# Optimization experiments

Hardware: AMD Instinct MI355X
Metric: run time of the kernel (lower is better)

## Reference

```python
import math
import jax, jax.numpy as jnp
import numpy as np

NUM_HEADS = 32
HEAD_DIM = 128
POOL = 16
MAX_REL = 8192
RMS_EPS = 1e-6


def _central_mask_features(distances, feature_size, seq_length):
    # center_widths = arange(F) + geomspace(1, seq_length-F+1, F, endpoint=False)
    log_end = math.log(float(seq_length - feature_size + 1))
    log_step = log_end / feature_size
    exponents = jnp.arange(feature_size, dtype=jnp.float32) * log_step
    center_widths = jnp.arange(feature_size, dtype=jnp.float32) + jnp.exp(exponents)
    return (center_widths > distances[..., None]).astype(jnp.float32)


def _shift(x, query_length, key_length):
    # x: [..., n_rows, n_diags] with n_diags = 2*n_rows
    batch_shape = x.shape[:-2]
    n_rows, n_diags = x.shape[-2], x.shape[-1]
    x = x.reshape(*batch_shape, n_diags, n_rows)
    x = x[..., 1:, :]
    x = x.reshape(*batch_shape, n_rows, n_diags - 1)
    return x[..., :key_length]


def setup_inputs() -> dict:
    key = jax.random.key(0)
    ks = jax.random.split(key, 12)
    B, S, D = 1, 8192, 1536
    HD = NUM_HEADS * HEAD_DIM  # 4096
    s = 0.02
    return {
        "x": jax.random.normal(ks[0], (B, S, D), jnp.float32),
        "w_rms": jnp.ones((D,), jnp.float32),
        "W_q": jax.random.normal(ks[1], (D, HD), jnp.float32) * s,
        "W_k": jax.random.normal(ks[2], (D, HD), jnp.float32) * s,
        "W_pos": jax.random.normal(ks[3], (2 * NUM_HEADS, HD), jnp.float32) * s,
        "b_pos": jnp.zeros((HD,), jnp.float32),
        "q_r_bias": jax.random.normal(ks[4], (1, 1, NUM_HEADS, HEAD_DIM), jnp.float32) * s,
        "k_r_bias": jax.random.normal(ks[5], (1, 1, NUM_HEADS, HEAD_DIM), jnp.float32) * s,
        "W_yq": jax.random.normal(ks[6], (D, HEAD_DIM), jnp.float32) * s,
        "W_yk": jax.random.normal(ks[7], (D, HEAD_DIM), jnp.float32) * s,
        "W_pair": jax.random.normal(ks[8], (NUM_HEADS, HEAD_DIM), jnp.float32) * s,
        "b_pair": jnp.zeros((HEAD_DIM,), jnp.float32),
    }


def reference(x, w_rms, W_q, W_k, W_pos, b_pos, q_r_bias, k_r_bias, W_yq, W_yk, W_pair, b_pair):
    B, S, D = x.shape
    Sp = S // POOL
    # mean-pool along sequence (kernel=stride=16)
    x_pooled = x.reshape(B, Sp, POOL, D).mean(axis=2)
    # RMSNorm
    x_norm = x_pooled * jax.lax.rsqrt(jnp.mean(x_pooled * x_pooled, axis=-1, keepdims=True) + RMS_EPS) * w_rms

    q = (x_norm @ W_q).reshape(B, Sp, NUM_HEADS, HEAD_DIM)
    k = (x_norm @ W_k).reshape(B, Sp, NUM_HEADS, HEAD_DIM)

    # relative-position features
    range_vec = jnp.arange(-Sp, Sp, dtype=jnp.float32)
    pos_feat = _central_mask_features(jnp.abs(range_vec), NUM_HEADS, MAX_REL // POOL)  # [2Sp, H]
    sign = jnp.sign(range_vec)[:, None]
    pos_feat = jnp.concatenate([pos_feat, sign * pos_feat], axis=-1)  # [2Sp, 2H]
    pos_enc = (pos_feat @ W_pos + b_pos).reshape(2 * Sp, NUM_HEADS, HEAD_DIM)

    term_q = jnp.einsum('bqhc,phc->bhqp', q + q_r_bias, pos_enc)
    term_k = jnp.einsum('bkhc,phc->bhkp', k + k_r_bias, pos_enc)
    rel_q_a = _shift(term_q, Sp, Sp)  # [B,H,Q,K]
    rel_k_a = _shift(term_k, Sp, Sp)
    rel_q_a = jnp.transpose(rel_q_a, (0, 2, 3, 1))  # [B,Q,K,H]
    rel_k_a = jnp.transpose(rel_k_a, (0, 3, 2, 1))  # [B,P,K,H]

    a = jnp.einsum('bqhc,bkhc->bqkh', q, k)
    a = a + 0.5 * (rel_q_a + rel_k_a)

    x_gelu = jax.nn.gelu(x_norm, approximate=False)
    y_q = x_gelu @ W_yq  # [B,Sp,HEAD_DIM]
    y_k = x_gelu @ W_yk

    pair_act = a @ W_pair + b_pair + y_q[:, :, None, :] + y_k[:, None, :, :]
    return pair_act
```

## Files before the change

kernel.cpp:

```cpp
#include <hip/hip_runtime.h>
#include <hip/hip_bf16.h>
#include <math.h>
#include <stdint.h>

#define NHEADS 32
#define HDIM 128
#define POOLW 16
#define DMODEL 1536
#define SPOOL 512
#define HDTOT 4096
#define PEROWS 1024
#define NPAIR (SPOOL * SPOOL)
#define TCOLS 80

typedef __hip_bfloat16 bf16;
typedef short short8 __attribute__((ext_vector_type(8)));
typedef float f32x4 __attribute__((ext_vector_type(4)));

__device__ __forceinline__ float b2f(const bf16 v) { return __bfloat162float(v); }
__device__ __forceinline__ bf16 f2b(float v) { return __float2bfloat16(v); }
__device__ __forceinline__ short f2bs(float v) {
  bf16 b = __float2bfloat16(v);
  return *reinterpret_cast<short*>(&b);
}

__device__ __forceinline__ void gload_lds16(const void* g, void* l) {
  const __attribute__((address_space(1))) uint32_t* gp =
      (const __attribute__((address_space(1))) uint32_t*)(uintptr_t)g;
  __attribute__((address_space(3))) uint32_t* lp =
      (__attribute__((address_space(3))) uint32_t*)(uintptr_t)l;
  __builtin_amdgcn_global_load_lds(gp, lp, 16, 0, 0);
}

__global__ __launch_bounds__(256) void pool_rms_gelu_bf(
    const float* __restrict__ x, const float* __restrict__ w_rms,
    bf16* __restrict__ xn, bf16* __restrict__ xg) {
  int sp = blockIdx.x;
  int tid = threadIdx.x;
  __shared__ float buf[DMODEL];
  __shared__ float red[256];
  const float* xrow = x + (size_t)sp * POOLW * DMODEL;
  float ss = 0.f;
  for (int d = tid; d < DMODEL; d += 256) {
    float s = 0.f;
#pragma unroll
    for (int p = 0; p < POOLW; ++p) s += xrow[p * DMODEL + d];
    s *= (1.0f / POOLW);
    buf[d] = s;
    ss += s * s;
  }
  red[tid] = ss;
  __syncthreads();
  for (int off = 128; off > 0; off >>= 1) {
    if (tid < off) red[tid] += red[tid + off];
    __syncthreads();
  }
  float rms = rsqrtf(red[0] / DMODEL + 1e-6f);
  for (int d = tid; d < DMODEL; d += 256) {
    float v = buf[d] * rms * w_rms[d];
    xn[(size_t)sp * DMODEL + d] = f2b(v);
    xg[(size_t)sp * DMODEL + d] = f2b(0.5f * v * (1.0f + erff(v * 0.70710678118654752f)));
  }
}

__global__ __launch_bounds__(256) void suffix_kernel(
    const float* __restrict__ W_pos, float* __restrict__ SW0, float* __restrict__ SW1) {
  int j = blockIdx.x * 256 + threadIdx.x;
  float s0 = 0.f, s1 = 0.f;
  SW0[32 * HDTOT + j] = 0.f;
  SW1[32 * HDTOT + j] = 0.f;
  for (int f = 31; f >= 0; --f) {
    s0 += W_pos[f * HDTOT + j];
    s1 += W_pos[(NHEADS + f) * HDTOT + j];
    SW0[f * HDTOT + j] = s0;
    SW1[f * HDTOT + j] = s1;
  }
}

__global__ __launch_bounds__(256) void prep_kernel(
    const float* __restrict__ SW0, const float* __restrict__ SW1,
    const float* __restrict__ b_pos, const float* __restrict__ qrb,
    const float* __restrict__ krb, bf16* __restrict__ SWb,
    float* __restrict__ RB, short* __restrict__ fm_tab) {
  int b = blockIdx.x, t = threadIdx.x;
  if (b < 32) {
    int h = b;
    bf16* dst = SWb + (size_t)h * 128 * 128;
    for (int rr = 0; rr < 128; rr += 2) {
      int g = rr + (t >> 7);
      int c = t & 127;
      float v;
      if (g < 33) v = SW0[(size_t)g * HDTOT + h * 128 + c];
      else if (g < 66) v = SW1[(size_t)(g - 33) * HDTOT + h * 128 + c];
      else if (g == 66) v = b_pos[h * 128 + c];
      else v = 0.f;
      dst[(size_t)g * 128 + c] = f2b(v);
    }
  } else if (b < 96) {
    int idx = b - 32;
    int s = idx >> 5, h = idx & 31;
    const float* rb = (s ? krb : qrb) + h * 128;
    if (t < 128) {
      int g = t;
      float acc = 0.f;
      if (g < 33) { for (int c = 0; c < 128; ++c) acc += rb[c] * SW0[(size_t)g * HDTOT + h * 128 + c]; }
      else if (g < 66) { for (int c = 0; c < 128; ++c) acc += rb[c] * SW1[(size_t)(g - 33) * HDTOT + h * 128 + c]; }
      else if (g == 66) { for (int c = 0; c < 128; ++c) acc += rb[c] * b_pos[h * 128 + c]; }
      RB[(size_t)idx * 128 + g] = acc;
    }
  } else {
    for (int p = t; p < 1024; p += 256) {
      float dist = fabsf((float)(p - 512));
      double ls = log(481.0) / 32.0;
      int fmv = 0;
      for (int f = 0; f < 32; ++f) {
        float cw = (float)f + expf((float)f * (float)ls);
        if (cw <= dist) fmv = f + 1;
      }
      fm_tab[p] = (short)fmv;
    }
  }
}

__global__ __launch_bounds__(256) void transpose_cast(
    const float* __restrict__ in, bf16* __restrict__ out, int R, int C) {
  __shared__ float tile[32][33];
  int c0 = blockIdx.x * 32, r0 = blockIdx.y * 32;
  int tx = threadIdx.x & 31, ty = threadIdx.x >> 5;
  for (int i = ty; i < 32; i += 8) tile[i][tx] = in[(size_t)(r0 + i) * C + c0 + tx];
  __syncthreads();
  for (int i = ty; i < 32; i += 8) out[(size_t)(c0 + i) * R + r0 + tx] = f2b(tile[tx][i]);
}

__global__ __launch_bounds__(256) void gemm_mfma(
    const bf16* __restrict__ A, int lda, long long batchA,
    const bf16* __restrict__ BT, int ldb, long long batchB,
    void* __restrict__ C, int ldc, long long batchC,
    const float* __restrict__ extra, int mode, int M, int N, int K) {
  __shared__ short Asub[128][32];
  __shared__ short Bsub[64][32];
  const int t = threadIdx.x;
  const int lane = t & 63;
  const int w = t >> 6;
  const int m0 = blockIdx.y * 128, n0 = blockIdx.x * 64;
  const int wm = (w >> 1) * 64, wn = (w & 1) * 32;
  const bf16* Ag = A + (size_t)blockIdx.z * batchA;
  const bf16* Bg = BT + (size_t)blockIdx.z * batchB;

  const int ar0 = t >> 2;
  const int as0 = t & 3;
  const int ao0 = as0 ^ (ar0 & 3);
  char* AsubB = (char*)&Asub[0][0];
  char* BsubB = (char*)&Bsub[0][0];
  char* ldsA0 = AsubB + w * 1024;
  char* ldsA1 = AsubB + 4096 + w * 1024;
  char* ldsB0 = BsubB + w * 1024;

  const int quad = lane >> 4, mr = lane & 15;
  f32x4 acc[4][2];
#pragma unroll
  for (int mi = 0; mi < 4; ++mi)
#pragma unroll
    for (int ni = 0; ni < 2; ++ni) acc[mi][ni] = (f32x4){0.f, 0.f, 0.f, 0.f};

  for (int k0 = 0; k0 < K; k0 += 32) {
    gload_lds16(Ag + (size_t)(m0 + ar0) * lda + k0 + ao0 * 8, ldsA0);
    gload_lds16(Ag + (size_t)(m0 + 64 + ar0) * lda + k0 + ao0 * 8, ldsA1);
    gload_lds16(Bg + (size_t)(n0 + ar0) * ldb + k0 + ao0 * 8, ldsB0);
    __syncthreads();
    short8 af[4];
#pragma unroll
    for (int mi = 0; mi < 4; ++mi) {
      int r = wm + mi * 16 + mr;
      af[mi] = *(const short8*)&Asub[r][(quad ^ (r & 3)) * 8];
    }
    short8 bfr[2];
#pragma unroll
    for (int ni = 0; ni < 2; ++ni) {
      int r = wn + ni * 16 + mr;
      bfr[ni] = *(const short8*)&Bsub[r][(quad ^ (r & 3)) * 8];
    }
#pragma unroll
    for (int mi = 0; mi < 4; ++mi)
#pragma unroll
      for (int ni = 0; ni < 2; ++ni)
        acc[mi][ni] = __builtin_amdgcn_mfma_f32_16x16x32_bf16(af[mi], bfr[ni], acc[mi][ni], 0, 0, 0);
    __syncthreads();
  }

  size_t cbase = (size_t)blockIdx.z * batchC;
#pragma unroll
  for (int mi = 0; mi < 4; ++mi) {
#pragma unroll
    for (int ni = 0; ni < 2; ++ni) {
#pragma unroll
      for (int r = 0; r < 4; ++r) {
        int gm = m0 + wm + mi * 16 + quad * 4 + r;
        int gn = n0 + wn + ni * 16 + mr;
        float v = acc[mi][ni][r];
        if (mode == 0) {
          ((float*)C)[cbase + (size_t)gm * ldc + gn] = v;
        } else if (mode == 1) {
          ((bf16*)C)[cbase + (size_t)gm * ldc + gn] = f2b(v);
        } else {
          if (gn < TCOLS) {
            ((float*)C)[cbase + (size_t)gm * ldc + gn] =
                v + extra[blockIdx.z * 128 + gn];
          }
        }
      }
    }
  }
}

#define MEGA_LDS 145536
__global__ __launch_bounds__(512) void mega_kernel(
    const bf16* __restrict__ QKp, const float* __restrict__ Tg,
    const short* __restrict__ fm_tab, const bf16* __restrict__ WpT,
    const float* __restrict__ b_pair, const float* __restrict__ yqk,
    float* __restrict__ out) {
  extern __shared__ char sm[];
  short* Qs = (short*)(sm);
  short* Ks = (short*)(sm + 8192);
  float* Ssc = (float*)(sm + 57344);
  short* fmL = (short*)(sm + 61568);
  short* Pl = (short*)(sm + 63616);

  const int t = threadIdx.x;
  const int lane = t & 63, w = t >> 6;
  const int quad = lane >> 4, mr = lane & 15;
  const int q0 = (blockIdx.x >> 4) * 32;
  const int k0 = (blockIdx.x & 15) * 32;

  const int c_ks = t >> 7;
  const int c_cc = t & 127;
  const int c_r = c_cc >> 2;
  const int c_pc = c_cc & 3;
  const int qk_col = c_ks * 32 + ((c_pc ^ (c_r & 3)) * 8);
  const int t_r0 = t / 20, t_p0 = t - t_r0 * 20;
  const int c2 = 512 + t;
  const int t_r1 = c2 / 20, t_p1 = c2 - t_r1 * 20;

#define STAGE_QK(h)                                                                   \
  {                                                                                   \
    gload_lds16(QKp + (size_t)(q0 + c_r) * 8192 + (h)*128 + qk_col, (char*)Qs + t * 16); \
    gload_lds16(QKp + (size_t)(k0 + c_r) * 8192 + 4096 + (h)*128 + qk_col,            \
                (char*)Ks + t * 16);                                                  \
  }
#define STAGE_T(h)                                                                    \
  {                                                                                   \
    char* dq = sm + 16384 + ((h)&1) * 10240;                                          \
    char* dk = sm + 36864 + ((h)&1) * 10240;                                          \
    const float* sq_ = Tg + (size_t)(h)*512 * TCOLS;                                  \
    const float* sk_ = Tg + (size_t)(32 + (h)) * 512 * TCOLS;                         \
    gload_lds16(sq_ + (size_t)(q0 + t_r0) * TCOLS + t_p0 * 4, dq + t * 16);           \
    gload_lds16(sk_ + (size_t)(k0 + t_r0) * TCOLS + t_p0 * 4, dk + t * 16);           \
    if (t < 128) {                                                                    \
      gload_lds16(sq_ + (size_t)(q0 + t_r1) * TCOLS + t_p1 * 4, dq + c2 * 16);        \
      gload_lds16(sk_ + (size_t)(k0 + t_r1) * TCOLS + t_p1 * 4, dk + c2 * 16);        \
    }                                                                                 \
  }

  if (t < 128) gload_lds16(fm_tab + t * 8, (char*)fmL + t * 16);
  STAGE_QK(0);
  STAGE_T(0);
  __syncthreads();

  for (int h = 0; h < 32; ++h) {
    if (w < 4) {
      const int smi = w >> 1, sni = w & 1;
      const int ra = smi * 16 + mr, rb = sni * 16 + mr;
      f32x4 accS = (f32x4){0.f, 0.f, 0.f, 0.f};
#pragma unroll
      for (int ks = 0; ks < 4; ++ks) {
        short8 af = *(const short8*)&Qs[ks * 1024 + ra * 32 + ((quad ^ (ra & 3)) * 8)];
        short8 bfv = *(const short8*)&Ks[ks * 1024 + rb * 32 + ((quad ^ (rb & 3)) * 8)];
        accS = __builtin_amdgcn_mfma_f32_16x16x32_bf16(af, bfv, accS, 0, 0, 0);
      }
#pragma unroll
      for (int r = 0; r < 4; ++r)
        Ssc[(smi * 16 + quad * 4 + r) * 33 + sni * 16 + mr] = accS[r];
    }
    __syncthreads();
    if (h < 31) {
      STAGE_QK(h + 1);
      STAGE_T(h + 1);
    }
    {
      const float* tq = (const float*)(sm + 16384 + (h & 1) * 10240);
      const float* tk = (const float*)(sm + 36864 + (h & 1) * 10240);
#pragma unroll
      for (int j = 0; j < 2; ++j) {
        int m = j * 512 + t;
        int qL = m >> 5, kL = m & 31;
        int pq = 512 + (k0 + kL) - (q0 + qL);
        int gq = fmL[pq], gk = fmL[1024 - pq];
        float sq = (pq > 512) ? 1.f : ((pq < 512) ? -1.f : 0.f);
        float vq = tq[qL * TCOLS + gq] + sq * tq[qL * TCOLS + 33 + gq] + tq[qL * TCOLS + 66];
        float vk = tk[kL * TCOLS + gk] - sq * tk[kL * TCOLS + 33 + gk] + tk[kL * TCOLS + 66];
        float val = Ssc[qL * 33 + kL] + 0.5f * (vq + vk);
        Pl[m * 40 + h] = f2bs(val);
      }
    }
    __syncthreads();
  }

  short8 bfr[8];
  float bp[8];
#pragma unroll
  for (int ni = 0; ni < 8; ++ni) {
    int c = ni * 16 + mr;
    bfr[ni] = *(const short8*)(WpT + (size_t)c * 32 + quad * 8);
    bp[ni] = b_pair[c];
  }
#pragma unroll
  for (int mi = 0; mi < 8; ++mi) {
    int mb = w * 128 + mi * 16;
    short8 af = *(const short8*)&Pl[(mb + mr) * 40 + quad * 8];
    f32x4 acc[8];
#pragma unroll
    for (int ni = 0; ni < 8; ++ni)
      acc[ni] = __builtin_amdgcn_mfma_f32_16x16x32_bf16(
          af, bfr[ni], (f32x4){0.f, 0.f, 0.f, 0.f}, 0, 0, 0);
#pragma unroll
    for (int r = 0; r < 4; ++r) {
      int m = mb + quad * 4 + r;
      int q = q0 + (m >> 5), k = k0 + (m & 31);
      const float* yq = yqk + (size_t)q * 256;
      const float* yk = yqk + (size_t)k * 256 + 128;
      float* orow = out + ((size_t)q * 512 + k) * 128;
#pragma unroll
      for (int ni = 0; ni < 8; ++ni) {
        int c = ni * 16 + mr;
        orow[c] = acc[ni][r] + bp[ni] + yq[c] + yk[c];
      }
    }
  }
}

extern "C" void kernel_launch(void* const* d_in, const int* in_sizes, int n_in,
                              void* d_out, int out_size, void* d_ws, size_t ws_size,
                              hipStream_t stream) {
  const float* x      = (const float*)d_in[0];
  const float* w_rms  = (const float*)d_in[1];
  const float* W_q    = (const float*)d_in[2];
  const float* W_k    = (const float*)d_in[3];
  const float* W_pos  = (const float*)d_in[4];
  const float* b_pos  = (const float*)d_in[5];
  const float* qrb    = (const float*)d_in[6];
  const float* krb    = (const float*)d_in[7];
  const float* W_yq   = (const float*)d_in[8];
  const float* W_yk   = (const float*)d_in[9];
  const float* W_pair = (const float*)d_in[10];
  const float* b_pair = (const float*)d_in[11];
  float* out = (float*)d_out;

  static bool attr_set = false;
  if (!attr_set) {
    (void)hipFuncSetAttribute((const void*)mega_kernel,
                              hipFuncAttributeMaxDynamicSharedMemorySize, MEGA_LDS);
    attr_set = true;
  }

  char* w = (char*)d_ws;
  bf16* xn   = (bf16*)w; w += (size_t)SPOOL * DMODEL * 2;
  bf16* xg   = (bf16*)w; w += (size_t)SPOOL * DMODEL * 2;
  bf16* QKp  = (bf16*)w; w += (size_t)SPOOL * 8192 * 2;
  float* yqk = (float*)w; w += (size_t)SPOOL * 256 * 4;
  bf16* yqkT = (bf16*)w; w += (size_t)256 * DMODEL * 2;
  bf16* WpT  = (bf16*)w; w += (size_t)HDIM * NHEADS * 2;
  float* SW0 = (float*)w; w += (size_t)33 * HDTOT * 4;
  float* SW1 = (float*)w; w += (size_t)33 * HDTOT * 4;
  bf16* SWb  = (bf16*)w; w += (size_t)NHEADS * 128 * 128 * 2;
  float* RB  = (float*)w; w += (size_t)64 * 128 * 4;
  short* fm_tab = (short*)w; w += 1024 * 2;
  w = (char*)(((uintptr_t)w + 255) & ~(uintptr_t)255);
  bf16* WqT = (bf16*)w; w += (size_t)HDTOT * DMODEL * 2;
  bf16* WkT = (bf16*)w; w += (size_t)HDTOT * DMODEL * 2;
  float* Tg = (float*)w; w += (size_t)2 * NHEADS * SPOOL * TCOLS * 4;

  pool_rms_gelu_bf<<<SPOOL, 256, 0, stream>>>(x, w_rms, xn, xg);
  suffix_kernel<<<HDTOT / 256, 256, 0, stream>>>(W_pos, SW0, SW1);
  prep_kernel<<<97, 256, 0, stream>>>(SW0, SW1, b_pos, qrb, krb, SWb, RB, fm_tab);
  transpose_cast<<<dim3(HDTOT / 32, DMODEL / 32), 256, 0, stream>>>(W_q, WqT, DMODEL, HDTOT);
  transpose_cast<<<dim3(HDTOT / 32, DMODEL / 32), 256, 0, stream>>>(W_k, WkT, DMODEL, HDTOT);
  transpose_cast<<<dim3(HDIM / 32, DMODEL / 32), 256, 0, stream>>>(W_yq, yqkT, DMODEL, HDIM);
  transpose_cast<<<dim3(HDIM / 32, DMODEL / 32), 256, 0, stream>>>(W_yk, yqkT + (size_t)HDIM * DMODEL, DMODEL, HDIM);
  transpose_cast<<<dim3(HDIM / 32, 1), 256, 0, stream>>>(W_pair, WpT, NHEADS, HDIM);
  gemm_mfma<<<dim3(8192 / 64, SPOOL / 128, 1), 256, 0, stream>>>(
      xn, DMODEL, 0, WqT, DMODEL, 0, QKp, 8192, 0, nullptr, 1, SPOOL, 8192, DMODEL);
  gemm_mfma<<<dim3(256 / 64, SPOOL / 128, 1), 256, 0, stream>>>(
      xg, DMODEL, 0, yqkT, DMODEL, 0, yqk, 256, 0, nullptr, 0, SPOOL, 256, DMODEL);
  gemm_mfma<<<dim3(128 / 64, SPOOL / 128, NHEADS), 256, 0, stream>>>(
      QKp, 8192, 128, SWb, 128, 128 * 128, Tg, TCOLS, (long long)SPOOL * TCOLS,
      RB, 5, SPOOL, 128, 128);
  gemm_mfma<<<dim3(128 / 64, SPOOL / 128, NHEADS), 256, 0, stream>>>(
      QKp + 4096, 8192, 128, SWb, 128, 128 * 128,
      Tg + (size_t)NHEADS * SPOOL * TCOLS, TCOLS, (long long)SPOOL * TCOLS,
      RB + 32 * 128, 5, SPOOL, 128, 128);
  mega_kernel<<<256, 512, MEGA_LDS, stream>>>(QKp, Tg, fm_tab, WpT, b_pair, yqk, out);
}
```

Baseline: 402.8 us.

## Fuse weight transpose-cast into projection GEMM and merge launches

Removes the separate transpose_cast kernels for W_q, W_k, W_yq, W_yk and W_pair. The projection GEMM now reads the fp32 weights directly, converts them to bf16 and stages them in LDS, and it computes both the QK and the y projections in a single launch. The two per-head table GEMMs are merged into one launch with 64 z-slices, and the W_pair transpose moves into prep_kernel. Index math that does not change across heads in mega_kernel is hoisted out of the head loop. The B-operand loads are now strided scalar fp32 reads instead of 16-byte async loads, so the GEMM main loop may become less efficient even though the transpose traffic and several launches are removed.

```diff
diff --git a/kernel.cpp b/kernel.cpp
--- a/kernel.cpp
+++ b/kernel.cpp
@@ -80,8 +80,9 @@
 __global__ __launch_bounds__(256) void prep_kernel(
     const float* __restrict__ SW0, const float* __restrict__ SW1,
     const float* __restrict__ b_pos, const float* __restrict__ qrb,
-    const float* __restrict__ krb, bf16* __restrict__ SWb,
-    float* __restrict__ RB, short* __restrict__ fm_tab) {
+    const float* __restrict__ krb, const float* __restrict__ W_pair,
+    bf16* __restrict__ SWb, float* __restrict__ RB, short* __restrict__ fm_tab,
+    bf16* __restrict__ WpT) {
   int b = blockIdx.x, t = threadIdx.x;
   if (b < 32) {
     int h = b;
@@ -108,7 +109,7 @@
       else if (g == 66) { for (int c = 0; c < 128; ++c) acc += rb[c] * b_pos[h * 128 + c]; }
       RB[(size_t)idx * 128 + g] = acc;
     }
-  } else {
+  } else if (b == 96) {
     for (int p = t; p < 1024; p += 256) {
       float dist = fabsf((float)(p - 512));
       double ls = log(481.0) / 32.0;
@@ -119,33 +120,124 @@
       }
       fm_tab[p] = (short)fmv;
     }
-  }
-}
-
-__global__ __launch_bounds__(256) void transpose_cast(
-    const float* __restrict__ in, bf16* __restrict__ out, int R, int C) {
-  __shared__ float tile[32][33];
-  int c0 = blockIdx.x * 32, r0 = blockIdx.y * 32;
-  int tx = threadIdx.x & 31, ty = threadIdx.x >> 5;
-  for (int i = ty; i < 32; i += 8) tile[i][tx] = in[(size_t)(r0 + i) * C + c0 + tx];
-  __syncthreads();
-  for (int i = ty; i < 32; i += 8) out[(size_t)(c0 + i) * R + r0 + tx] = f2b(tile[tx][i]);
-}
-
-__global__ __launch_bounds__(256) void gemm_mfma(
-    const bf16* __restrict__ A, int lda, long long batchA,
-    const bf16* __restrict__ BT, int ldb, long long batchB,
-    void* __restrict__ C, int ldc, long long batchC,
-    const float* __restrict__ extra, int mode, int M, int N, int K) {
+  } else {
+    for (int idx = t; idx < NHEADS * HDIM; idx += 256) {
+      int c = idx >> 5, h = idx & 31;
+      WpT[(size_t)c * 32 + h] = f2b(W_pair[h * HDIM + c]);
+    }
+  }
+}
+
+__global__ __launch_bounds__(256) void gemm_proj(
+    const bf16* __restrict__ xn, const bf16* __restrict__ xg,
+    const float* __restrict__ W_q, const float* __restrict__ W_k,
+    const float* __restrict__ W_yq, const float* __restrict__ W_yk,
+    bf16* __restrict__ QKp, float* __restrict__ yqk) {
+  __shared__ short Asub[128][32];
+  __shared__ short Bsub[64][40];
+  const int t = threadIdx.x;
+  const int lane = t & 63;
+  const int w = t >> 6;
+  const int bx = blockIdx.x;
+  const int m0 = blockIdx.y * 128;
+  const int wm = (w >> 1) * 64, wn = (w & 1) * 32;
+
+  const bf16* A;
+  const float* Wb;
+  int ncol, ldw;
+  if (bx < 128) {
+    A = xn;
+    int n0 = bx * 64;
+    if (n0 < 4096) { Wb = W_q; ncol = n0; } else { Wb = W_k; ncol = n0 - 4096; }
+    ldw = 4096;
+  } else {
+    A = xg;
+    int x2 = bx - 128;
+    int n0 = x2 * 64;
+    if (n0 < 128) { Wb = W_yq; ncol = n0; } else { Wb = W_yk; ncol = n0 - 128; }
+    ldw = 128;
+  }
+
+  const int ar0 = t >> 2;
+  const int as0 = t & 3;
+  const int ao0 = as0 ^ (ar0 & 3);
+  char* AsubB = (char*)&Asub[0][0];
+  char* ldsA0 = AsubB + w * 1024;
+  char* ldsA1 = AsubB + 4096 + w * 1024;
+
+  const int bn = t & 63;
+  const int bkg = t >> 6;
+
+  const int quad = lane >> 4, mr = lane & 15;
+  f32x4 acc[4][2];
+#pragma unroll
+  for (int mi = 0; mi < 4; ++mi)
+#pragma unroll
+    for (int ni = 0; ni < 2; ++ni) acc[mi][ni] = (f32x4){0.f, 0.f, 0.f, 0.f};
+
+  for (int k0 = 0; k0 < DMODEL; k0 += 32) {
+    gload_lds16(A + (size_t)(m0 + ar0) * DMODEL + k0 + ao0 * 8, ldsA0);
+    gload_lds16(A + (size_t)(m0 + 64 + ar0) * DMODEL + k0 + ao0 * 8, ldsA1);
+    {
+      short8 bs;
+#pragma unroll
+      for (int j = 0; j < 8; ++j)
+        bs[j] = f2bs(Wb[(size_t)(k0 + bkg * 8 + j) * ldw + ncol + bn]);
+      *(short8*)&Bsub[bn][bkg * 8] = bs;
+    }
+    __syncthreads();
+    short8 af[4];
+#pragma unroll
+    for (int mi = 0; mi < 4; ++mi) {
+      int r = wm + mi * 16 + mr;
+      af[mi] = *(const short8*)&Asub[r][(quad ^ (r & 3)) * 8];
+    }
+    short8 bfr[2];
+#pragma unroll
+    for (int ni = 0; ni < 2; ++ni) {
+      int r = wn + ni * 16 + mr;
+      bfr[ni] = *(const short8*)&Bsub[r][quad * 8];
+    }
+#pragma unroll
+    for (int mi = 0; mi < 4; ++mi)
+#pragma unroll
+      for (int ni = 0; ni < 2; ++ni)
+        acc[mi][ni] = __builtin_amdgcn_mfma_f32_16x16x32_bf16(af[mi], bfr[ni], acc[mi][ni], 0, 0, 0);
+    __syncthreads();
+  }
+
+#pragma unroll
+  for (int mi = 0; mi < 4; ++mi) {
+#pragma unroll
+    for (int ni = 0; ni < 2; ++ni) {
+#pragma unroll
+      for (int r = 0; r < 4; ++r) {
+        int gm = m0 + wm + mi * 16 + quad * 4 + r;
+        int gnl = wn + ni * 16 + mr;
+        float v = acc[mi][ni][r];
+        if (bx < 128) {
+          QKp[(size_t)gm * 8192 + bx * 64 + gnl] = f2b(v);
+        } else {
+          yqk[(size_t)gm * 256 + (bx - 128) * 64 + gnl] = v;
+        }
+      }
+    }
+  }
+}
+
+__global__ __launch_bounds__(256) void gemm_table(
+    const bf16* __restrict__ QKp, const bf16* __restrict__ SWb,
+    const float* __restrict__ RB, float* __restrict__ Tg) {
   __shared__ short Asub[128][32];
   __shared__ short Bsub[64][32];
   const int t = threadIdx.x;
   const int lane = t & 63;
   const int w = t >> 6;
+  const int z = blockIdx.z;
   const int m0 = blockIdx.y * 128, n0 = blockIdx.x * 64;
   const int wm = (w >> 1) * 64, wn = (w & 1) * 32;
-  const bf16* Ag = A + (size_t)blockIdx.z * batchA;
-  const bf16* Bg = BT + (size_t)blockIdx.z * batchB;
+  const bf16* Ag = QKp + (size_t)(z >> 5) * 4096 + (size_t)(z & 31) * 128;
+  const bf16* Bg = SWb + (size_t)(z & 31) * 128 * 128;
 
   const int ar0 = t >> 2;
   const int as0 = t & 3;
@@ -163,10 +255,10 @@
 #pragma unroll
     for (int ni = 0; ni < 2; ++ni) acc[mi][ni] = (f32x4){0.f, 0.f, 0.f, 0.f};
 
-  for (int k0 = 0; k0 < K; k0 += 32) {
-    gload_lds16(Ag + (size_t)(m0 + ar0) * lda + k0 + ao0 * 8, ldsA0);
-    gload_lds16(Ag + (size_t)(m0 + 64 + ar0) * lda + k0 + ao0 * 8, ldsA1);
-    gload_lds16(Bg + (size_t)(n0 + ar0) * ldb + k0 + ao0 * 8, ldsB0);
+  for (int k0 = 0; k0 < 128; k0 += 32) {
+    gload_lds16(Ag + (size_t)(m0 + ar0) * 8192 + k0 + ao0 * 8, ldsA0);
+    gload_lds16(Ag + (size_t)(m0 + 64 + ar0) * 8192 + k0 + ao0 * 8, ldsA1);
+    gload_lds16(Bg + (size_t)(n0 + ar0) * 128 + k0 + ao0 * 8, ldsB0);
     __syncthreads();
     short8 af[4];
 #pragma unroll
@@ -188,7 +280,8 @@
     __syncthreads();
   }
 
-  size_t cbase = (size_t)blockIdx.z * batchC;
+  float* Cz = Tg + (size_t)z * 512 * TCOLS;
+  const float* ex = RB + (size_t)z * 128;
 #pragma unroll
   for (int mi = 0; mi < 4; ++mi) {
 #pragma unroll
@@ -197,17 +290,7 @@
       for (int r = 0; r < 4; ++r) {
         int gm = m0 + wm + mi * 16 + quad * 4 + r;
         int gn = n0 + wn + ni * 16 + mr;
-        float v = acc[mi][ni][r];
-        if (mode == 0) {
-          ((float*)C)[cbase + (size_t)gm * ldc + gn] = v;
-        } else if (mode == 1) {
-          ((bf16*)C)[cbase + (size_t)gm * ldc + gn] = f2b(v);
-        } else {
-          if (gn < TCOLS) {
-            ((float*)C)[cbase + (size_t)gm * ldc + gn] =
-                v + extra[blockIdx.z * 128 + gn];
-          }
-        }
+        if (gn < TCOLS) Cz[(size_t)gm * TCOLS + gn] = acc[mi][ni][r] + ex[gn];
       }
     }
   }
@@ -266,6 +349,25 @@
   STAGE_T(0);
   __syncthreads();
 
+  int tqa[2], tqb[2], tqc[2], tka[2], tkb[2], tkc[2], ssco[2], plo[2];
+  float sgn[2];
+#pragma unroll
+  for (int j = 0; j < 2; ++j) {
+    int m = j * 512 + t;
+    int qL = m >> 5, kL = m & 31;
+    int pq = 512 + (k0 + kL) - (q0 + qL);
+    int gq = fmL[pq], gk = fmL[1024 - pq];
+    sgn[j] = (pq > 512) ? 1.f : ((pq < 512) ? -1.f : 0.f);
+    tqa[j] = qL * TCOLS + gq;
+    tqb[j] = qL * TCOLS + 33 + gq;
+    tqc[j] = qL * TCOLS + 66;
+    tka[j] = kL * TCOLS + gk;
+    tkb[j] = kL * TCOLS + 33 + gk;
+    tkc[j] = kL * TCOLS + 66;
+    ssco[j] = qL * 33 + kL;
+    plo[j] = m * 40;
+  }
+
   for (int h = 0; h < 32; ++h) {
     if (w < 4) {
       const int smi = w >> 1, sni = w & 1;
@@ -291,15 +393,10 @@
       const float* tk = (const float*)(sm + 36864 + (h & 1) * 10240);
 #pragma unroll
       for (int j = 0; j < 2; ++j) {
-        int m = j * 512 + t;
-        int qL = m >> 5, kL = m & 31;
-        int pq = 512 + (k0 + kL) - (q0 + qL);
-        int gq = fmL[pq], gk = fmL[1024 - pq];
-        float sq = (pq > 512) ? 1.f : ((pq < 512) ? -1.f : 0.f);
-        float vq = tq[qL * TCOLS + gq] + sq * tq[qL * TCOLS + 33 + gq] + tq[qL * TCOLS + 66];
-        float vk = tk[kL * TCOLS + gk] - sq * tk[kL * TCOLS + 33 + gk] + tk[kL * TCOLS + 66];
-        float val = Ssc[qL * 33 + kL] + 0.5f * (vq + vk);
-        Pl[m * 40 + h] = f2bs(val);
+        float vq = tq[tqa[j]] + sgn[j] * tq[tqb[j]] + tq[tqc[j]];
+        float vk = tk[tka[j]] - sgn[j] * tk[tkb[j]] + tk[tkc[j]];
+        float val = Ssc[ssco[j]] + 0.5f * (vq + vk);
+        Pl[plo[j] + h] = f2bs(val);
       }
     }
     __syncthreads();
@@ -367,7 +464,6 @@
   bf16* xg   = (bf16*)w; w += (size_t)SPOOL * DMODEL * 2;
   bf16* QKp  = (bf16*)w; w += (size_t)SPOOL * 8192 * 2;
   float* yqk = (float*)w; w += (size_t)SPOOL * 256 * 4;
-  bf16* yqkT = (bf16*)w; w += (size_t)256 * DMODEL * 2;
   bf16* WpT  = (bf16*)w; w += (size_t)HDIM * NHEADS * 2;
   float* SW0 = (float*)w; w += (size_t)33 * HDTOT * 4;
   float* SW1 = (float*)w; w += (size_t)33 * HDTOT * 4;
@@ -375,28 +471,14 @@
   float* RB  = (float*)w; w += (size_t)64 * 128 * 4;
   short* fm_tab = (short*)w; w += 1024 * 2;
   w = (char*)(((uintptr_t)w + 255) & ~(uintptr_t)255);
-  bf16* WqT = (bf16*)w; w += (size_t)HDTOT * DMODEL * 2;
-  bf16* WkT = (bf16*)w; w += (size_t)HDTOT * DMODEL * 2;
   float* Tg = (float*)w; w += (size_t)2 * NHEADS * SPOOL * TCOLS * 4;
 
   pool_rms_gelu_bf<<<SPOOL, 256, 0, stream>>>(x, w_rms, xn, xg);
   suffix_kernel<<<HDTOT / 256, 256, 0, stream>>>(W_pos, SW0, SW1);
-  prep_kernel<<<97, 256, 0, stream>>>(SW0, SW1, b_pos, qrb, krb, SWb, RB, fm_tab);
-  transpose_cast<<<dim3(HDTOT / 32, DMODEL / 32), 256, 0, stream>>>(W_q, WqT, DMODEL, HDTOT);
-  transpose_cast<<<dim3(HDTOT / 32, DMODEL / 32), 256, 0, stream>>>(W_k, WkT, DMODEL, HDTOT);
-  transpose_cast<<<dim3(HDIM / 32, DMODEL / 32), 256, 0, stream>>>(W_yq, yqkT, DMODEL, HDIM);
-  transpose_cast<<<dim3(HDIM / 32, DMODEL / 32), 256, 0, stream>>>(W_yk, yqkT + (size_t)HDIM * DMODEL, DMODEL, HDIM);
-  transpose_cast<<<dim3(HDIM / 32, 1), 256, 0, stream>>>(W_pair, WpT, NHEADS, HDIM);
-  gemm_mfma<<<dim3(8192 / 64, SPOOL / 128, 1), 256, 0, stream>>>(
-      xn, DMODEL, 0, WqT, DMODEL, 0, QKp, 8192, 0, nullptr, 1, SPOOL, 8192, DMODEL);
-  gemm_mfma<<<dim3(256 / 64, SPOOL / 128, 1), 256, 0, stream>>>(
-      xg, DMODEL, 0, yqkT, DMODEL, 0, yqk, 256, 0, nullptr, 0, SPOOL, 256, DMODEL);
-  gemm_mfma<<<dim3(128 / 64, SPOOL / 128, NHEADS), 256, 0, stream>>>(
-      QKp, 8192, 128, SWb, 128, 128 * 128, Tg, TCOLS, (long long)SPOOL * TCOLS,
-      RB, 5, SPOOL, 128, 128);
-  gemm_mfma<<<dim3(128 / 64, SPOOL / 128, NHEADS), 256, 0, stream>>>(
-      QKp + 4096, 8192, 128, SWb, 128, 128 * 128,
-      Tg + (size_t)NHEADS * SPOOL * TCOLS, TCOLS, (long long)SPOOL * TCOLS,
-      RB + 32 * 128, 5, SPOOL, 128, 128);
+  prep_kernel<<<98, 256, 0, stream>>>(SW0, SW1, b_pos, qrb, krb, W_pair,
+                                      SWb, RB, fm_tab, WpT);
+  gemm_proj<<<dim3(132, SPOOL / 128), 256, 0, stream>>>(
+      xn, xg, W_q, W_k, W_yq, W_yk, QKp, yqk);
+  gemm_table<<<dim3(128 / 64, SPOOL / 128, 64), 256, 0, stream>>>(QKp, SWb, RB, Tg);
   mega_kernel<<<256, 512, MEGA_LDS, stream>>>(QKp, Tg, fm_tab, WpT, b_pair, yqk, out);
 }
```

Result: faster. 344.5 us (-14.5%).
